# Optimization experiments

Measured on AMD Instinct MI355X. Metric: run time of the kernel, lower is better.

Reference implementation:

```python
import jax, jax.numpy as jnp
import numpy as np


def _window_indices(L, K):
    # 0-based (emo, cau) index pairs kept in the torch flattening order:
    # emo varies slowly (outer), cau varies fast (inner), |cau-emo| <= K.
    i = np.repeat(np.arange(L), L)
    j = np.tile(np.arange(L), L)
    m = np.abs(j - i) <= K
    return i[m], j[m]


def setup_inputs() -> dict:
    key = jax.random.key(0)
    ks = jax.random.split(key, 6)
    B, L, D = 4, 512, 768
    K, P = 10, 50
    R = 2 * D + P  # rank_feat_dim = 1586
    return {
        "doc_sents_h": jax.random.normal(ks[0], (B, L, D), jnp.float32),
        "pos_emb": jax.random.normal(ks[1], (2 * K + 1, P), jnp.float32) * 0.05,
        "W1": jax.random.normal(ks[2], (R, R), jnp.float32) * (1.0 / np.sqrt(R)),
        "b1": jax.random.normal(ks[3], (R,), jnp.float32) * 0.01,
        "W2": jax.random.normal(ks[4], (R, 1), jnp.float32) * (1.0 / np.sqrt(R)),
        "b2": jax.random.normal(ks[5], (1,), jnp.float32) * 0.01,
    }


def reference(doc_sents_h, pos_emb, W1, b1, W2, b2):
    B, L, D = doc_sents_h.shape
    K = (pos_emb.shape[0] - 1) // 2
    ei, ci = _window_indices(L, K)           # static numpy, shape [n]
    rel = jnp.asarray(ci - ei)               # [n] in [-K, K]
    # windowed pair features, [B, n, 2D] (skips the O(L^2) materialization)
    P_pairs = jnp.concatenate([doc_sents_h[:, ei], doc_sents_h[:, ci]], axis=-1)
    emb = pos_emb[rel + K]                   # [n, pos_dim]
    relf = rel.astype(pos_emb.dtype)
    kernel = jnp.exp(-jnp.square(relf[:, None] - relf[None, :]))  # [n, n]
    emb = kernel @ emb                       # [n, pos_dim], batch-invariant
    couples = jnp.concatenate(
        [P_pairs, jnp.broadcast_to(emb, (B,) + emb.shape)], axis=-1)  # [B, n, R]
    h = jax.nn.relu(couples @ W1 + b1)       # [B, n, R]
    pred = (h @ W2 + b2)[..., 0]             # [B, n]
    emo_cau_pos = jnp.stack(
        [jnp.asarray(ei) + 1, jnp.asarray(ci) + 1], axis=1)  # [n, 2], 1-based
    return pred, emo_cau_pos, h
```

## Files before the change

kernel.cpp:

```cpp
#include <hip/hip_runtime.h>
#include <math.h>

#define B_   4
#define L_   512
#define D_   768
#define K_   10
#define P_   50
#define R_   1586
#define NP_  10642
#define MROWS 2048
#define NPAD 1664

#define PRED_OFF 0
#define POS_OFF  (B_ * NP_)
#define H_OFF    (B_ * NP_ + NP_ * 2)

typedef __attribute__((ext_vector_type(8))) short short8;
typedef __attribute__((ext_vector_type(4))) float floatx4;

__device__ __forceinline__ unsigned short f2bf(float f) {
    union { float f; unsigned int u; } a; a.f = f;
    unsigned int u = a.u;
    return (unsigned short)((u + 0x7FFF + ((u >> 16) & 1)) >> 16);
}

__device__ __forceinline__ int pair_offset(int i) {
    int h = i < K_ ? i : K_;
    int off = h * (K_ + 1) + (h * (h - 1)) / 2;
    if (i > K_) {
        int fullEnd = i < (L_ - K_) ? i : (L_ - K_);
        off += (fullEnd - K_) * (2 * K_ + 1);
        if (i > L_ - K_) {
            int t = i - (L_ - K_);
            int first = 2 * K_;
            int last = L_ + K_ - (i - 1);
            off += (first + last) * t / 2;
        }
    }
    return off;
}

__global__ __launch_bounds__(256) void convert_A(
        const float* __restrict__ doc, unsigned short* __restrict__ At) {
    int idx = (blockIdx.x * 256 + threadIdx.x) * 4;
    float4 v = *(const float4*)(doc + idx);
    ushort4 o;
    o.x = f2bf(v.x); o.y = f2bf(v.y); o.z = f2bf(v.z); o.w = f2bf(v.w);
    *(ushort4*)(At + idx) = o;
}

__global__ __launch_bounds__(256) void convert_W(
        const float* __restrict__ W1, unsigned short* __restrict__ Wt) {
    int z = blockIdx.z;
    int k0 = blockIdx.x * 32;
    int n0 = blockIdx.y * 32;
    __shared__ float tile[32][33];
    int tx = threadIdx.x & 31, ty = threadIdx.x >> 5;
    #pragma unroll
    for (int r = 0; r < 4; ++r) {
        int k = k0 + ty + r * 8;
        int n = n0 + tx;
        tile[ty + r * 8][tx] = (n < R_) ? W1[(size_t)(z * D_ + k) * R_ + n] : 0.f;
    }
    __syncthreads();
    #pragma unroll
    for (int r = 0; r < 4; ++r) {
        int n = n0 + ty + r * 8;
        int k = k0 + tx;
        Wt[(size_t)z * NPAD * D_ + (size_t)n * D_ + k] = f2bf(tile[tx][ty + r * 8]);
    }
}

__global__ __launch_bounds__(256) void build_F(
        const float* __restrict__ pos_emb, const float* __restrict__ W1,
        const float* __restrict__ b1, float* __restrict__ F) {
    int s = blockIdx.x;
    __shared__ float Es[P_];
    if (threadIdx.x < P_) {
        float acc = 0.f;
        #pragma unroll
        for (int r = 0; r <= 2 * K_; ++r) {
            float cnt = (float)(L_ - (r > K_ ? r - K_ : K_ - r));
            float d = (float)(s - r);
            acc += cnt * expf(-d * d) * pos_emb[r * P_ + threadIdx.x];
        }
        Es[threadIdx.x] = acc;
    }
    __syncthreads();
    for (int j = threadIdx.x; j < R_; j += blockDim.x) {
        float acc = b1[j];
        #pragma unroll 10
        for (int p = 0; p < P_; ++p)
            acc += Es[p] * W1[(2 * D_ + p) * R_ + j];
        F[s * R_ + j] = acc;
    }
}

#define GLOAD_LDS16(g, l) __builtin_amdgcn_global_load_lds( \
    (const __attribute__((address_space(1))) void*)(g), \
    (__attribute__((address_space(3))) void*)(l), 16, 0, 0)

__global__ __launch_bounds__(256) void gemm_mfma(
        const unsigned short* __restrict__ At,
        const unsigned short* __restrict__ Wt,
        float* __restrict__ U, float* __restrict__ V) {
    __shared__ unsigned short Alds[128 * 32];
    __shared__ unsigned short Blds[128 * 32];
    const int tileN = blockIdx.x * 128;
    const int tileM = blockIdx.y * 128;
    const unsigned short* Bt = Wt + (size_t)blockIdx.z * NPAD * D_;
    float* C = blockIdx.z ? V : U;

    const int lane = threadIdx.x & 63;
    const int w = threadIdx.x >> 6;
    const int wm = (w & 1) * 64, wn = (w >> 1) * 64;
    const int quad = lane >> 4, l16 = lane & 15;

    floatx4 acc[4][4] = {};

    for (int k0 = 0; k0 < D_; k0 += 32) {
        #pragma unroll
        for (int t = 0; t < 2; ++t) {
            int g = (t * 4 + w) * 64 + lane;
            int m = g >> 2, c = g & 3;
            GLOAD_LDS16(At + (size_t)(tileM + m) * D_ + k0 + c * 8,
                        Alds + (t * 4 + w) * 512);
            GLOAD_LDS16(Bt + (size_t)(tileN + m) * D_ + k0 + c * 8,
                        Blds + (t * 4 + w) * 512);
        }
        __syncthreads();
        short8 a[4], b[4];
        #pragma unroll
        for (int im = 0; im < 4; ++im)
            a[im] = *(const short8*)&Alds[(wm + im * 16 + l16) * 32 + quad * 8];
        #pragma unroll
        for (int in = 0; in < 4; ++in)
            b[in] = *(const short8*)&Blds[(wn + in * 16 + l16) * 32 + quad * 8];
        #pragma unroll
        for (int im = 0; im < 4; ++im)
            #pragma unroll
            for (int in = 0; in < 4; ++in)
                acc[im][in] = __builtin_amdgcn_mfma_f32_16x16x32_bf16(
                    a[im], b[in], acc[im][in], 0, 0, 0);
        __syncthreads();
    }
    #pragma unroll
    for (int im = 0; im < 4; ++im) {
        #pragma unroll
        for (int in = 0; in < 4; ++in) {
            int col = tileN + wn + in * 16 + l16;
            if (col < R_) {
                #pragma unroll
                for (int r = 0; r < 4; ++r) {
                    int row = tileM + wm + im * 16 + quad * 4 + r;
                    C[(size_t)row * R_ + col] = acc[im][in][r];
                }
            }
        }
    }
}

#define NC2 13
__global__ __launch_bounds__(256) void epilogue(
        const float* __restrict__ U, const float* __restrict__ V,
        const float* __restrict__ F, const float* __restrict__ W2,
        const float* __restrict__ b2, float* __restrict__ out) {
    const int w    = threadIdx.x >> 6;
    const int lane = threadIdx.x & 63;
    const int i    = blockIdx.x * 4 + w;
    const int b    = blockIdx.y;

    const float2* u2  = (const float2*)(U + (size_t)(b * L_ + i) * R_);
    const float2* w2v = (const float2*)W2;

    float2 ur[NC2], wr[NC2];
    #pragma unroll
    for (int t = 0; t < NC2; ++t) {
        int c = lane + t * 64;
        if (c < R_ / 2) { ur[t] = u2[c]; wr[t] = w2v[c]; }
    }

    const int base = i - K_ > 0 ? i - K_ : 0;
    const int poff = pair_offset(i);
    const float bias = b2[0];

    for (int dj = 0; dj < 21; ++dj) {
        int j = i - K_ + dj;
        if (j < 0 || j >= L_) continue;
        int p = poff + (j - base);
        const float2* v2 = (const float2*)(V + (size_t)(b * L_ + j) * R_);
        const float2* f2 = (const float2*)(F + (size_t)dj * R_);
        float2* h2 = (float2*)(out + H_OFF + (size_t)(b * NP_ + p) * R_);

        float acc = 0.f;
        #pragma unroll
        for (int t = 0; t < NC2; ++t) {
            int c = lane + t * 64;
            if (c < R_ / 2) {
                float2 vv = v2[c], ff = f2[c];
                float h0 = fmaxf(ur[t].x + vv.x + ff.x, 0.f);
                float h1 = fmaxf(ur[t].y + vv.y + ff.y, 0.f);
                h2[c] = make_float2(h0, h1);
                acc += h0 * wr[t].x + h1 * wr[t].y;
            }
        }
        #pragma unroll
        for (int off = 32; off; off >>= 1) acc += __shfl_down(acc, off, 64);
        if (lane == 0) {
            out[PRED_OFF + b * NP_ + p] = acc + bias;
            if (b == 0) {
                out[POS_OFF + p * 2 + 0] = (float)(i + 1);
                out[POS_OFF + p * 2 + 1] = (float)(j + 1);
            }
        }
    }
}

extern "C" void kernel_launch(void* const* d_in, const int* in_sizes, int n_in,
                              void* d_out, int out_size, void* d_ws, size_t ws_size,
                              hipStream_t stream) {
    const float* doc     = (const float*)d_in[0];
    const float* pos_emb = (const float*)d_in[1];
    const float* W1      = (const float*)d_in[2];
    const float* b1      = (const float*)d_in[3];
    const float* W2      = (const float*)d_in[4];
    const float* b2      = (const float*)d_in[5];
    float* out = (float*)d_out;

    char* ws = (char*)d_ws;
    float* U = (float*)ws;
    float* V = U + (size_t)MROWS * R_;
    float* F = V + (size_t)MROWS * R_;
    size_t off = ((size_t)MROWS * R_ * 2 + (size_t)21 * R_) * 4;
    off = (off + 255) & ~(size_t)255;
    unsigned short* At = (unsigned short*)(ws + off);
    off += (size_t)MROWS * D_ * 2;
    off = (off + 255) & ~(size_t)255;
    unsigned short* Wt = (unsigned short*)(ws + off);

    convert_A<<<MROWS * D_ / 1024, 256, 0, stream>>>(doc, At);
    convert_W<<<dim3(D_ / 32, NPAD / 32, 2), 256, 0, stream>>>(W1, Wt);
    build_F<<<21, 256, 0, stream>>>(pos_emb, W1, b1, F);
    gemm_mfma<<<dim3(NPAD / 128, MROWS / 128, 2), 256, 0, stream>>>(At, Wt, U, V);
    epilogue<<<dim3(L_ / 4, B_), 256, 0, stream>>>(U, V, F, W2, b2, out);
}
```

Measured before the change: 372.0 us.

## Store U/V/F intermediates in bf16, split epilogue over two grid halves, nontemporal h stores

The GEMM partial products U and V and the positional term F are now stored as bf16 with a padded row stride instead of fp32. This halves the intermediate traffic read by the epilogue. The epilogue grid gains a z dimension that splits the 21 window offsets into two halves, doubling parallelism. The large h output is written with nontemporal stores to avoid polluting cache. It adds extra bf16 rounding error to h and pred.

```diff
diff --git a/kernel.cpp b/kernel.cpp
--- a/kernel.cpp
+++ b/kernel.cpp
@@ -10,6 +10,7 @@
 #define NP_  10642
 #define MROWS 2048
 #define NPAD 1664
+#define UVS  1600
 
 #define PRED_OFF 0
 #define POS_OFF  (B_ * NP_)
@@ -22,6 +23,10 @@
     union { float f; unsigned int u; } a; a.f = f;
     unsigned int u = a.u;
     return (unsigned short)((u + 0x7FFF + ((u >> 16) & 1)) >> 16);
+}
+__device__ __forceinline__ float bf2f(unsigned short u) {
+    union { unsigned int u; float f; } a; a.u = ((unsigned int)u) << 16;
+    return a.f;
 }
 
 __device__ __forceinline__ int pair_offset(int i) {
@@ -73,7 +78,7 @@
 
 __global__ __launch_bounds__(256) void build_F(
         const float* __restrict__ pos_emb, const float* __restrict__ W1,
-        const float* __restrict__ b1, float* __restrict__ F) {
+        const float* __restrict__ b1, unsigned short* __restrict__ Fb) {
     int s = blockIdx.x;
     __shared__ float Es[P_];
     if (threadIdx.x < P_) {
@@ -92,7 +97,7 @@
         #pragma unroll 10
         for (int p = 0; p < P_; ++p)
             acc += Es[p] * W1[(2 * D_ + p) * R_ + j];
-        F[s * R_ + j] = acc;
+        Fb[s * UVS + j] = f2bf(acc);
     }
 }
 
@@ -103,13 +108,13 @@
 __global__ __launch_bounds__(256) void gemm_mfma(
         const unsigned short* __restrict__ At,
         const unsigned short* __restrict__ Wt,
-        float* __restrict__ U, float* __restrict__ V) {
+        unsigned short* __restrict__ U, unsigned short* __restrict__ V) {
     __shared__ unsigned short Alds[128 * 32];
     __shared__ unsigned short Blds[128 * 32];
     const int tileN = blockIdx.x * 128;
     const int tileM = blockIdx.y * 128;
     const unsigned short* Bt = Wt + (size_t)blockIdx.z * NPAD * D_;
-    float* C = blockIdx.z ? V : U;
+    unsigned short* C = blockIdx.z ? V : U;
 
     const int lane = threadIdx.x & 63;
     const int w = threadIdx.x >> 6;
@@ -153,7 +158,7 @@
                 #pragma unroll
                 for (int r = 0; r < 4; ++r) {
                     int row = tileM + wm + im * 16 + quad * 4 + r;
-                    C[(size_t)row * R_ + col] = acc[im][in][r];
+                    C[(size_t)row * UVS + col] = f2bf(acc[im][in][r]);
                 }
             }
         }
@@ -162,45 +167,54 @@
 
 #define NC2 13
 __global__ __launch_bounds__(256) void epilogue(
-        const float* __restrict__ U, const float* __restrict__ V,
-        const float* __restrict__ F, const float* __restrict__ W2,
+        const unsigned short* __restrict__ U, const unsigned short* __restrict__ V,
+        const unsigned short* __restrict__ Fb, const float* __restrict__ W2,
         const float* __restrict__ b2, float* __restrict__ out) {
     const int w    = threadIdx.x >> 6;
     const int lane = threadIdx.x & 63;
     const int i    = blockIdx.x * 4 + w;
     const int b    = blockIdx.y;
-
-    const float2* u2  = (const float2*)(U + (size_t)(b * L_ + i) * R_);
-    const float2* w2v = (const float2*)W2;
+    const int half = blockIdx.z;
+
+    const ushort2* u2  = (const ushort2*)(U + (size_t)(b * L_ + i) * UVS);
+    const float2*  w2v = (const float2*)W2;
 
     float2 ur[NC2], wr[NC2];
     #pragma unroll
     for (int t = 0; t < NC2; ++t) {
         int c = lane + t * 64;
-        if (c < R_ / 2) { ur[t] = u2[c]; wr[t] = w2v[c]; }
+        if (c < R_ / 2) {
+            ushort2 uu = u2[c];
+            ur[t] = make_float2(bf2f(uu.x), bf2f(uu.y));
+            wr[t] = w2v[c];
+        }
     }
 
     const int base = i - K_ > 0 ? i - K_ : 0;
     const int poff = pair_offset(i);
     const float bias = b2[0];
-
-    for (int dj = 0; dj < 21; ++dj) {
+    const int dj0 = half ? 11 : 0;
+    const int dj1 = half ? 21 : 11;
+
+    for (int dj = dj0; dj < dj1; ++dj) {
         int j = i - K_ + dj;
         if (j < 0 || j >= L_) continue;
         int p = poff + (j - base);
-        const float2* v2 = (const float2*)(V + (size_t)(b * L_ + j) * R_);
-        const float2* f2 = (const float2*)(F + (size_t)dj * R_);
-        float2* h2 = (float2*)(out + H_OFF + (size_t)(b * NP_ + p) * R_);
+        const ushort2* v2 = (const ushort2*)(V + (size_t)(b * L_ + j) * UVS);
+        const ushort2* f2 = (const ushort2*)(Fb + (size_t)dj * UVS);
+        double* h2 = (double*)(out + H_OFF + (size_t)(b * NP_ + p) * R_);
 
         float acc = 0.f;
         #pragma unroll
         for (int t = 0; t < NC2; ++t) {
             int c = lane + t * 64;
             if (c < R_ / 2) {
-                float2 vv = v2[c], ff = f2[c];
-                float h0 = fmaxf(ur[t].x + vv.x + ff.x, 0.f);
-                float h1 = fmaxf(ur[t].y + vv.y + ff.y, 0.f);
-                h2[c] = make_float2(h0, h1);
+                ushort2 vv = v2[c], ff = f2[c];
+                float h0 = fmaxf(ur[t].x + bf2f(vv.x) + bf2f(ff.x), 0.f);
+                float h1 = fmaxf(ur[t].y + bf2f(vv.y) + bf2f(ff.y), 0.f);
+                union { float2 f; double d; } pk;
+                pk.f = make_float2(h0, h1);
+                __builtin_nontemporal_store(pk.d, h2 + c);
                 acc += h0 * wr[t].x + h1 * wr[t].y;
             }
         }
@@ -228,19 +242,18 @@
     float* out = (float*)d_out;
 
     char* ws = (char*)d_ws;
-    float* U = (float*)ws;
-    float* V = U + (size_t)MROWS * R_;
-    float* F = V + (size_t)MROWS * R_;
-    size_t off = ((size_t)MROWS * R_ * 2 + (size_t)21 * R_) * 4;
+    size_t off = 0;
+    unsigned short* U  = (unsigned short*)(ws + off); off += (size_t)MROWS * UVS * 2;
+    unsigned short* V  = (unsigned short*)(ws + off); off += (size_t)MROWS * UVS * 2;
+    unsigned short* Fb = (unsigned short*)(ws + off); off += (size_t)21 * UVS * 2;
     off = (off + 255) & ~(size_t)255;
-    unsigned short* At = (unsigned short*)(ws + off);
-    off += (size_t)MROWS * D_ * 2;
+    unsigned short* At = (unsigned short*)(ws + off); off += (size_t)MROWS * D_ * 2;
     off = (off + 255) & ~(size_t)255;
     unsigned short* Wt = (unsigned short*)(ws + off);
 
     convert_A<<<MROWS * D_ / 1024, 256, 0, stream>>>(doc, At);
     convert_W<<<dim3(D_ / 32, NPAD / 32, 2), 256, 0, stream>>>(W1, Wt);
-    build_F<<<21, 256, 0, stream>>>(pos_emb, W1, b1, F);
+    build_F<<<21, 256, 0, stream>>>(pos_emb, W1, b1, Fb);
     gemm_mfma<<<dim3(NPAD / 128, MROWS / 128, 2), 256, 0, stream>>>(At, Wt, U, V);
-    epilogue<<<dim3(L_ / 4, B_), 256, 0, stream>>>(U, V, F, W2, b2, out);
-}
+    epilogue<<<dim3(L_ / 4, B_, 2), 256, 0, stream>>>(U, V, Fb, W2, b2, out);
+}
```

After: 370.4 us. No clear change (-0.4%).
